# Performance work log

Measured on AMD Instinct MI355X. Metric: run time of the kernel, lower is better.

## Reference

```python
import jax, jax.numpy as jnp
import numpy as np

B, EMB, HID, OUT = 4096, 128, 512, 64
N_SUBPOLICIES = 5
STEPS = N_SUBPOLICIES * 4


def setup_inputs() -> dict:
    key = jax.random.key(0)
    ks = jax.random.split(key, 8)
    s = lambda k, shape: (jax.random.normal(k, shape, jnp.float32) * 0.05)
    return {
        "x": jax.random.randint(ks[0], (B,), 0, OUT),          # initial tokens
        "embedding": s(ks[1], (OUT, EMB)),                      # nn.Embedding weight
        "W_ih": s(ks[2], (4 * HID, EMB)),                       # LSTM input weights (i,f,g,o)
        "W_hh": s(ks[3], (4 * HID, HID)),                       # LSTM recurrent weights
        "b_ih": s(ks[4], (4 * HID,)),
        "b_hh": s(ks[5], (4 * HID,)),
        "W_lin": s(ks[6], (OUT, HID)),                          # nn.Linear weight
        "b_lin": s(ks[7], (OUT,)),
    }


def reference(x, embedding, W_ih, W_hh, b_ih, b_hh, W_lin, b_lin):
    keys = jax.random.split(jax.random.key(42), STEPS)
    h0 = jnp.zeros((x.shape[0], HID), jnp.float32)
    c0 = jnp.zeros_like(h0)
    b = b_ih + b_hh  # fold both LSTM biases once

    def step(carry, k):
        tok, h, c = carry
        e = embedding[tok]                               # [B, EMB]
        gates = e @ W_ih.T + h @ W_hh.T + b              # [B, 4H], torch gate order i,f,g,o
        i, f, g, o = jnp.split(gates, 4, axis=-1)
        c = jax.nn.sigmoid(f) * c + jax.nn.sigmoid(i) * jnp.tanh(g)
        h = jax.nn.sigmoid(o) * jnp.tanh(c)
        logits = h @ W_lin.T + b_lin                     # [B, OUT]
        probs = jax.nn.softmax(logits, axis=-1)
        # torch.multinomial(probs, 1) == categorical sample from logits
        new_tok = jax.random.categorical(k, logits, axis=-1)
        return (new_tok, h, c), probs

    _, probs = jax.lax.scan(step, (x, h0, c0), keys)     # [STEPS, B, OUT]
    return jnp.transpose(probs, (1, 0, 2))               # [B, STEPS, OUT]
```

## Files before the change

kernel.cpp:

```cpp
#include <hip/hip_runtime.h>
#include <stdint.h>
#include <math.h>


#define B_SZ  4096
#define EMB   128
#define HID   512
#define NOUT  64
#define STEPS 20
#define G4    2048
#define HF    ((size_t)B_SZ * HID)

typedef __attribute__((ext_vector_type(8)))  short bf16x8;
typedef __attribute__((ext_vector_type(16))) float f32x16;

union B8 { uint2 q[2]; bf16x8 v; };

__device__ __forceinline__ void tf2x32(uint32_t k0, uint32_t k1,
                                       uint32_t x0, uint32_t x1,
                                       uint32_t& o0, uint32_t& o1) {
  const uint32_t ks2 = k0 ^ k1 ^ 0x1BD11BDAu;
#define TFR(r) { x0 += x1; x1 = (x1 << (r)) | (x1 >> (32 - (r))); x1 ^= x0; }
  x0 += k0; x1 += k1;
  TFR(13) TFR(15) TFR(26) TFR(6)
  x0 += k1;  x1 += ks2 + 1u;
  TFR(17) TFR(29) TFR(16) TFR(24)
  x0 += ks2; x1 += k0 + 2u;
  TFR(13) TFR(15) TFR(26) TFR(6)
  x0 += k0;  x1 += k1 + 3u;
  TFR(17) TFR(29) TFR(16) TFR(24)
  x0 += k1;  x1 += ks2 + 4u;
  TFR(13) TFR(15) TFR(26) TFR(6)
  x0 += ks2; x1 += k0 + 5u;
#undef TFR
  o0 = x0; o1 = x1;
}

__device__ __forceinline__ void bf16split(float f, ushort& hi, ushort& lo) {
  uint32_t u = __float_as_uint(f);
  uint32_t r = u + 0x7fffu + ((u >> 16) & 1u);
  hi = (ushort)(r >> 16);
  float fh = __uint_as_float((r >> 16) << 16);
  float fl = f - fh;
  uint32_t v = __float_as_uint(fl);
  uint32_t r2 = v + 0x7fffu + ((v >> 16) & 1u);
  lo = (ushort)(r2 >> 16);
}

__device__ __forceinline__ void gload_lds16(const ushort* g, ushort* d) {
  __builtin_amdgcn_global_load_lds(
      (const __attribute__((address_space(1))) void*)g,
      (__attribute__((address_space(3))) void*)d, 16, 0, 0);
}

__global__ __launch_bounds__(256) void eproj_kernel(
    const float* __restrict__ emb, const float* __restrict__ W_ih,
    const float* __restrict__ b_ih, const float* __restrict__ b_hh,
    float* __restrict__ E) {
  const int t = blockIdx.x;
  __shared__ float es[EMB];
  for (int k = threadIdx.x; k < EMB; k += blockDim.x) es[k] = emb[t * EMB + k];
  __syncthreads();
  for (int j = threadIdx.x; j < G4; j += blockDim.x) {
    const float* w = W_ih + (size_t)j * EMB;
    float acc = 0.f;
#pragma unroll 8
    for (int k = 0; k < EMB; k += 4) {
      float4 wv = *(const float4*)(w + k);
      acc += wv.x * es[k] + wv.y * es[k + 1] + wv.z * es[k + 2] + wv.w * es[k + 3];
    }
    E[(size_t)t * G4 + j] = acc + b_ih[j] + b_hh[j];
  }
}

__global__ __launch_bounds__(256) void wprep_whh(
    const float* __restrict__ W_hh, ushort* __restrict__ wswz) {
  const int id = blockIdx.x * 256 + threadIdx.x;
  const int ub    = id >> 14;
  const int w14   = id & 16383;
  const int kt    = w14 >> 11;
  const int plane = (w14 >> 10) & 1;
  const int row   = (w14 >> 3) & 127;
  const int ec    = w14 & 7;
  const int grow = (row >> 5) * HID + ub * 32 + (row & 31);
  const int swz = (row & 15) << 2;
  ushort vals[8];
#pragma unroll
  for (int j = 0; j < 8; ++j) {
    const int e = ec * 8 + j;
    const int k = kt * 64 + (e ^ swz);
    ushort hi, lo;
    bf16split(W_hh[(size_t)grow * HID + k], hi, lo);
    vals[j] = plane ? lo : hi;
  }
  *(uint4*)(wswz + (size_t)id * 8) = *(const uint4*)vals;
}

__global__ __launch_bounds__(256) void wprep_lin(
    const float* __restrict__ W_lin, float* __restrict__ wlt) {
  const int id = blockIdx.x * 256 + threadIdx.x;
  const int j = id & 3, o = (id >> 2) & 63, k4 = id >> 8;
  wlt[id] = W_lin[(size_t)o * HID + k4 * 4 + j];
}

__global__ __launch_bounds__(512, 2) void lstm_step_mfma(
    const ushort* __restrict__ hf,
    float*        __restrict__ c,
    float*        __restrict__ h_out,
    ushort*       __restrict__ hf_out,
    const ushort* __restrict__ wswz,
    const float*  __restrict__ E,
    const int*    __restrict__ tok,
    int zh)
{
  __shared__ ushort Bt[2][16384];
  const int tid = threadIdx.x;
  const int w = tid >> 6, l = tid & 63;
  const int l31 = l & 31, lh = l >> 5;

  const int raw = blockIdx.x;
  const int x = raw & 7, j = raw >> 3;
  const int ub  = (x & 3) * 4 + (j & 3);
  const int mbi = (x >> 2) * 8 + (j >> 2);
  const int m0 = mbi * 256 + w * 32;
  const int u0 = ub * 32;

  f32x16 acc[4] = {};

  const size_t abase = ((size_t)(m0 >> 5) * 64 + lh) * 256 + (size_t)l31 * 8;
  const ushort* a0 = hf + abase;
  const ushort* a1 = hf + HF + abase;
  const ushort* wsrc = wswz + (size_t)ub * 131072 + (size_t)(w * 512 + l * 8);

  if (!zh) {
    bf16x8 Aa0[4], Aa1[4], Ab0[4], Ab1[4];

#define SB0 __builtin_amdgcn_sched_barrier(0)
#define STAGE(KT, BUF) { \
  _Pragma("unroll") \
  for (int r = 0; r < 4; ++r) \
    gload_lds16(wsrc + (size_t)(KT) * 16384 + r * 4096, &Bt[BUF][w * 512 + r * 4096]); }
#define LOADA(KT, A0v, A1v) { \
  _Pragma("unroll") \
  for (int kc = 0; kc < 4; ++kc) { \
    const size_t ko = (size_t)((KT) * 8 + kc * 2) * 256; \
    A0v[kc] = *(const bf16x8*)(a0 + ko); \
    A1v[kc] = *(const bf16x8*)(a1 + ko); } }
#define COMPUTE(BUF, A0v, A1v) { \
  __builtin_amdgcn_s_setprio(1); \
  _Pragma("unroll") \
  for (int kc = 0; kc < 4; ++kc) { \
    _Pragma("unroll") \
    for (int s = 0; s < 4; ++s) { \
      const int row = s * 32 + l31; \
      const int swz = (row & 15) << 2; \
      const int eb = kc * 16 + lh * 8; \
      const ushort* rb = &Bt[BUF][row * 64]; \
      B8 uh, ul; \
      uh.q[0] = *(const uint2*)(rb + ((eb)     ^ swz)); \
      uh.q[1] = *(const uint2*)(rb + ((eb + 4) ^ swz)); \
      ul.q[0] = *(const uint2*)(rb + 8192 + ((eb)     ^ swz)); \
      ul.q[1] = *(const uint2*)(rb + 8192 + ((eb + 4) ^ swz)); \
      acc[s] = __builtin_amdgcn_mfma_f32_32x32x16_bf16(A0v[kc], uh.v, acc[s], 0, 0, 0); \
      acc[s] = __builtin_amdgcn_mfma_f32_32x32x16_bf16(A1v[kc], uh.v, acc[s], 0, 0, 0); \
      acc[s] = __builtin_amdgcn_mfma_f32_32x32x16_bf16(A0v[kc], ul.v, acc[s], 0, 0, 0); } } \
  __builtin_amdgcn_s_setprio(0); }
#define FENCE8 { asm volatile("s_waitcnt vmcnt(8)" ::: "memory"); SB0; \
                 __builtin_amdgcn_s_barrier(); }

    STAGE(0, 0); SB0; LOADA(0, Aa0, Aa1); SB0;
    FENCE8;
    STAGE(1, 1); SB0; LOADA(1, Ab0, Ab1); SB0;
    COMPUTE(0, Aa0, Aa1); FENCE8;
    STAGE(2, 0); SB0; LOADA(2, Aa0, Aa1); SB0;
    COMPUTE(1, Ab0, Ab1); FENCE8;
    STAGE(3, 1); SB0; LOADA(3, Ab0, Ab1); SB0;
    COMPUTE(0, Aa0, Aa1); FENCE8;
    STAGE(4, 0); SB0; LOADA(4, Aa0, Aa1); SB0;
    COMPUTE(1, Ab0, Ab1); FENCE8;
    STAGE(5, 1); SB0; LOADA(5, Ab0, Ab1); SB0;
    COMPUTE(0, Aa0, Aa1); FENCE8;
    STAGE(6, 0); SB0; LOADA(6, Aa0, Aa1); SB0;
    COMPUTE(1, Ab0, Ab1); FENCE8;
    STAGE(7, 1); SB0; LOADA(7, Ab0, Ab1); SB0;
    COMPUTE(0, Aa0, Aa1); FENCE8;
    COMPUTE(1, Ab0, Ab1);
#undef FENCE8
#undef COMPUTE
#undef LOADA
#undef STAGE
#undef SB0
  }

  const int u = u0 + l31;
#pragma unroll
  for (int r = 0; r < 16; ++r) {
    const int m = m0 + (r & 3) + 8 * (r >> 2) + 4 * lh;
    const int tk = tok[m];
    const float* Erow = E + (size_t)tk * G4;
    const float gi = acc[0][r] + Erow[u];
    const float gf = acc[1][r] + Erow[HID + u];
    const float gg = acc[2][r] + Erow[2 * HID + u];
    const float go = acc[3][r] + Erow[3 * HID + u];
    const float si = 1.f / (1.f + expf(-gi));
    const float sf = 1.f / (1.f + expf(-gf));
    const float so = 1.f / (1.f + expf(-go));
    const size_t ci = (size_t)m * HID + u;
    const float cv = zh ? 0.f : c[ci];
    const float nc = sf * cv + si * tanhf(gg);
    const float hv = so * tanhf(nc);
    c[ci] = nc;
    h_out[ci] = hv;
    ushort hi, lo;
    bf16split(hv, hi, lo);
    const size_t fo = ((size_t)(m >> 5) * 64 + (u >> 3)) * 256 + (size_t)(m & 31) * 8 + (u & 7);
    hf_out[fo] = hi;
    hf_out[HF + fo] = lo;
  }
}

__global__ __launch_bounds__(256) void logits2(
    const float* __restrict__ h, const float* __restrict__ wlt,
    const float* __restrict__ b_lin, float* __restrict__ out,
    int* __restrict__ tok, int step)
{
  const int tid = threadIdx.x;
  const int o = tid & 63;
  const int rg = tid >> 6;
  const int b0 = blockIdx.x * 8 + rg * 2;
  float acc0 = 0.f, acc1 = 0.f;
  const float* h0 = h + (size_t)b0 * HID;
  const float* h1 = h0 + HID;
#pragma unroll 4
  for (int k4 = 0; k4 < 128; ++k4) {
    const float4 wv = *(const float4*)(wlt + (size_t)(k4 * 64 + o) * 4);
    const float4 x0 = *(const float4*)(h0 + k4 * 4);
    const float4 x1 = *(const float4*)(h1 + k4 * 4);
    acc0 += wv.x * x0.x + wv.y * x0.y + wv.z * x0.z + wv.w * x0.w;
    acc1 += wv.x * x1.x + wv.y * x1.y + wv.z * x1.z + wv.w * x1.w;
  }
  const float bl = b_lin[o];
  uint32_t s0, s1;
  tf2x32(0u, 42u, 0u, (uint32_t)step, s0, s1);
  float lg[2] = {acc0 + bl, acc1 + bl};
#pragma unroll
  for (int r = 0; r < 2; ++r) {
    const int b = b0 + r;
    const float logit = lg[r];
    float mx = logit;
#pragma unroll
    for (int d = 32; d; d >>= 1) mx = fmaxf(mx, __shfl_xor(mx, d));
    float e = expf(logit - mx);
    float ssum = e;
#pragma unroll
    for (int d = 32; d; d >>= 1) ssum += __shfl_xor(ssum, d);
    out[((size_t)b * STEPS + step) * NOUT + o] = e / ssum;

    uint32_t r0, r1;
    tf2x32(s0, s1, 0u, (uint32_t)(b * NOUT + o), r0, r1);
    const uint32_t bits = r0 ^ r1;
    float uu = __uint_as_float((bits >> 9) | 0x3f800000u) - 1.0f;
    uu = fmaxf(uu, 1.17549435e-38f);
    const float gmb = -logf(-logf(uu));
    float v = logit + gmb;
    int bi = o;
#pragma unroll
    for (int d = 32; d; d >>= 1) {
      float ov = __shfl_xor(v, d);
      int oi = __shfl_xor(bi, d);
      if (ov > v || (ov == v && oi < bi)) { v = ov; bi = oi; }
    }
    if (o == 0) tok[b] = bi;
  }
}

extern "C" void kernel_launch(void* const* d_in, const int* in_sizes, int n_in,
                              void* d_out, int out_size, void* d_ws, size_t ws_size,
                              hipStream_t stream) {
  const int*   x     = (const int*)d_in[0];
  const float* emb   = (const float*)d_in[1];
  const float* W_ih  = (const float*)d_in[2];
  const float* W_hh  = (const float*)d_in[3];
  const float* b_ih  = (const float*)d_in[4];
  const float* b_hh  = (const float*)d_in[5];
  const float* W_lin = (const float*)d_in[6];
  const float* b_lin = (const float*)d_in[7];
  float* out = (float*)d_out;

  float*  E    = (float*)d_ws;
  float*  c    = E + 131072;
  float*  h    = c + HF;
  float*  wlt  = h + HF;
  ushort* hf0  = (ushort*)(wlt + 32768);
  ushort* hf1  = hf0 + 2 * HF;
  ushort* wswz = hf1 + 2 * HF;
  int*    tok  = (int*)(wswz + 2097152);

  eproj_kernel<<<64, 256, 0, stream>>>(emb, W_ih, b_ih, b_hh, E);
  wprep_whh<<<1024, 256, 0, stream>>>(W_hh, wswz);
  wprep_lin<<<128, 256, 0, stream>>>(W_lin, wlt);

  const int* cur_tok = x;
  ushort* hfin = hf0;
  ushort* hfout = hf1;
  for (int t = 0; t < STEPS; ++t) {
    lstm_step_mfma<<<256, 512, 0, stream>>>(hfin, c, h, hfout, wswz, E, cur_tok, t == 0);
    logits2<<<512, 256, 0, stream>>>(h, wlt, b_lin, out, tok, t);
    cur_tok = tok;
    ushort* tmp = hfin; hfin = hfout; hfout = tmp;
  }
}
```

Before: 1.326 ms.

## Fuse all LSTM steps and logits into one persistent kernel with grid barriers

Replaces the 40 per-step kernel launches (LSTM step plus logits/sampling) with a single persistent kernel of 256 blocks. Blocks synchronise through a global atomic grid barrier, and the cell state now lives in registers instead of global memory. Sigmoid and tanh switch to fast exp/rcp approximations. This removes launch overhead and the c-state round trips. In exchange it depends on all 256 blocks being co-resident, adds two grid barriers per step, and the approximate activations may change numerics slightly.

```diff
diff --git a/kernel.cpp b/kernel.cpp
--- a/kernel.cpp
+++ b/kernel.cpp
@@ -10,6 +10,7 @@
 #define STEPS 20
 #define G4    2048
 #define HF    ((size_t)B_SZ * HID)
+#define NBLK  256
 
 typedef __attribute__((ext_vector_type(8)))  short bf16x8;
 typedef __attribute__((ext_vector_type(16))) float f32x16;
@@ -53,6 +54,31 @@
       (__attribute__((address_space(3))) void*)d, 16, 0, 0);
 }
 
+__device__ __forceinline__ float fsig(float x) {
+  return __builtin_amdgcn_rcpf(1.f + __expf(-x));
+}
+__device__ __forceinline__ float ftanh(float x) {
+  return 1.f - 2.f * __builtin_amdgcn_rcpf(1.f + __expf(2.f * x));
+}
+
+__device__ __forceinline__ void gridbar(unsigned* cnt, unsigned* gen) {
+  __syncthreads();
+  if (threadIdx.x == 0) {
+    __threadfence();
+    unsigned g = __hip_atomic_load(gen, __ATOMIC_RELAXED, __HIP_MEMORY_SCOPE_AGENT);
+    unsigned a = __hip_atomic_fetch_add(cnt, 1u, __ATOMIC_ACQ_REL, __HIP_MEMORY_SCOPE_AGENT);
+    if (a == NBLK - 1) {
+      __hip_atomic_store(cnt, 0u, __ATOMIC_RELAXED, __HIP_MEMORY_SCOPE_AGENT);
+      __hip_atomic_fetch_add(gen, 1u, __ATOMIC_RELEASE, __HIP_MEMORY_SCOPE_AGENT);
+    } else {
+      while (__hip_atomic_load(gen, __ATOMIC_ACQUIRE, __HIP_MEMORY_SCOPE_AGENT) == g)
+        __builtin_amdgcn_s_sleep(2);
+    }
+  }
+  __syncthreads();
+  __threadfence();
+}
+
 __global__ __launch_bounds__(256) void eproj_kernel(
     const float* __restrict__ emb, const float* __restrict__ W_ih,
     const float* __restrict__ b_ih, const float* __restrict__ b_hh,
@@ -103,15 +129,18 @@
   wlt[id] = W_lin[(size_t)o * HID + k4 * 4 + j];
 }
 
-__global__ __launch_bounds__(512, 2) void lstm_step_mfma(
-    const ushort* __restrict__ hf,
-    float*        __restrict__ c,
-    float*        __restrict__ h_out,
-    ushort*       __restrict__ hf_out,
+__global__ __launch_bounds__(512, 2) void ctrl_persist(
+    const int*    __restrict__ x,
     const ushort* __restrict__ wswz,
     const float*  __restrict__ E,
-    const int*    __restrict__ tok,
-    int zh)
+    const float*  __restrict__ wlt,
+    const float*  __restrict__ b_lin,
+    float*        __restrict__ h_out,
+    ushort*       __restrict__ hf0,
+    ushort*       __restrict__ hf1,
+    int*          __restrict__ tok,
+    float*        __restrict__ out,
+    unsigned*     __restrict__ bar)
 {
   __shared__ ushort Bt[2][16384];
   const int tid = threadIdx.x;
@@ -119,27 +148,36 @@
   const int l31 = l & 31, lh = l >> 5;
 
   const int raw = blockIdx.x;
-  const int x = raw & 7, j = raw >> 3;
-  const int ub  = (x & 3) * 4 + (j & 3);
-  const int mbi = (x >> 2) * 8 + (j >> 2);
+  const int xq = raw & 7, jq = raw >> 3;
+  const int ub  = (xq & 3) * 4 + (jq & 3);
+  const int mbi = (xq >> 2) * 8 + (jq >> 2);
   const int m0 = mbi * 256 + w * 32;
   const int u0 = ub * 32;
-
-  f32x16 acc[4] = {};
-
-  const size_t abase = ((size_t)(m0 >> 5) * 64 + lh) * 256 + (size_t)l31 * 8;
-  const ushort* a0 = hf + abase;
-  const ushort* a1 = hf + HF + abase;
+  const int u  = u0 + l31;
+
   const ushort* wsrc = wswz + (size_t)ub * 131072 + (size_t)(w * 512 + l * 8);
-
-  if (!zh) {
-    bf16x8 Aa0[4], Aa1[4], Ab0[4], Ab1[4];
+  const int lb0 = raw * 16 + w * 2;
+
+  f32x16 creg = {};
+
+  for (int t = 0; t < STEPS; ++t) {
+    const ushort* hin  = (t & 1) ? hf1 : hf0;
+    ushort*       hout = (t & 1) ? hf0 : hf1;
+    const int*    tk   = t ? tok : x;
+
+    f32x16 acc[4] = {};
+
+    if (t > 0) {
+      const size_t abase = ((size_t)(m0 >> 5) * 64 + lh) * 256 + (size_t)l31 * 8;
+      const ushort* a0 = hin + abase;
+      const ushort* a1 = hin + HF + abase;
+      bf16x8 Aa0[4], Aa1[4], Ab0[4], Ab1[4];
 
 #define SB0 __builtin_amdgcn_sched_barrier(0)
 #define STAGE(KT, BUF) { \
   _Pragma("unroll") \
-  for (int r = 0; r < 4; ++r) \
-    gload_lds16(wsrc + (size_t)(KT) * 16384 + r * 4096, &Bt[BUF][w * 512 + r * 4096]); }
+  for (int rr = 0; rr < 4; ++rr) \
+    gload_lds16(wsrc + (size_t)(KT) * 16384 + rr * 4096, &Bt[BUF][w * 512 + rr * 4096]); }
 #define LOADA(KT, A0v, A1v) { \
   _Pragma("unroll") \
   for (int kc = 0; kc < 4; ++kc) { \
@@ -168,109 +206,104 @@
 #define FENCE8 { asm volatile("s_waitcnt vmcnt(8)" ::: "memory"); SB0; \
                  __builtin_amdgcn_s_barrier(); }
 
-    STAGE(0, 0); SB0; LOADA(0, Aa0, Aa1); SB0;
-    FENCE8;
-    STAGE(1, 1); SB0; LOADA(1, Ab0, Ab1); SB0;
-    COMPUTE(0, Aa0, Aa1); FENCE8;
-    STAGE(2, 0); SB0; LOADA(2, Aa0, Aa1); SB0;
-    COMPUTE(1, Ab0, Ab1); FENCE8;
-    STAGE(3, 1); SB0; LOADA(3, Ab0, Ab1); SB0;
-    COMPUTE(0, Aa0, Aa1); FENCE8;
-    STAGE(4, 0); SB0; LOADA(4, Aa0, Aa1); SB0;
-    COMPUTE(1, Ab0, Ab1); FENCE8;
-    STAGE(5, 1); SB0; LOADA(5, Ab0, Ab1); SB0;
-    COMPUTE(0, Aa0, Aa1); FENCE8;
-    STAGE(6, 0); SB0; LOADA(6, Aa0, Aa1); SB0;
-    COMPUTE(1, Ab0, Ab1); FENCE8;
-    STAGE(7, 1); SB0; LOADA(7, Ab0, Ab1); SB0;
-    COMPUTE(0, Aa0, Aa1); FENCE8;
-    COMPUTE(1, Ab0, Ab1);
+      STAGE(0, 0); SB0; LOADA(0, Aa0, Aa1); SB0;
+      FENCE8;
+      STAGE(1, 1); SB0; LOADA(1, Ab0, Ab1); SB0;
+      COMPUTE(0, Aa0, Aa1); FENCE8;
+      STAGE(2, 0); SB0; LOADA(2, Aa0, Aa1); SB0;
+      COMPUTE(1, Ab0, Ab1); FENCE8;
+      STAGE(3, 1); SB0; LOADA(3, Ab0, Ab1); SB0;
+      COMPUTE(0, Aa0, Aa1); FENCE8;
+      STAGE(4, 0); SB0; LOADA(4, Aa0, Aa1); SB0;
+      COMPUTE(1, Ab0, Ab1); FENCE8;
+      STAGE(5, 1); SB0; LOADA(5, Ab0, Ab1); SB0;
+      COMPUTE(0, Aa0, Aa1); FENCE8;
+      STAGE(6, 0); SB0; LOADA(6, Aa0, Aa1); SB0;
+      COMPUTE(1, Ab0, Ab1); FENCE8;
+      STAGE(7, 1); SB0; LOADA(7, Ab0, Ab1); SB0;
+      COMPUTE(0, Aa0, Aa1); FENCE8;
+      COMPUTE(1, Ab0, Ab1);
 #undef FENCE8
 #undef COMPUTE
 #undef LOADA
 #undef STAGE
 #undef SB0
-  }
-
-  const int u = u0 + l31;
-#pragma unroll
-  for (int r = 0; r < 16; ++r) {
-    const int m = m0 + (r & 3) + 8 * (r >> 2) + 4 * lh;
-    const int tk = tok[m];
-    const float* Erow = E + (size_t)tk * G4;
-    const float gi = acc[0][r] + Erow[u];
-    const float gf = acc[1][r] + Erow[HID + u];
-    const float gg = acc[2][r] + Erow[2 * HID + u];
-    const float go = acc[3][r] + Erow[3 * HID + u];
-    const float si = 1.f / (1.f + expf(-gi));
-    const float sf = 1.f / (1.f + expf(-gf));
-    const float so = 1.f / (1.f + expf(-go));
-    const size_t ci = (size_t)m * HID + u;
-    const float cv = zh ? 0.f : c[ci];
-    const float nc = sf * cv + si * tanhf(gg);
-    const float hv = so * tanhf(nc);
-    c[ci] = nc;
-    h_out[ci] = hv;
-    ushort hi, lo;
-    bf16split(hv, hi, lo);
-    const size_t fo = ((size_t)(m >> 5) * 64 + (u >> 3)) * 256 + (size_t)(m & 31) * 8 + (u & 7);
-    hf_out[fo] = hi;
-    hf_out[HF + fo] = lo;
-  }
-}
-
-__global__ __launch_bounds__(256) void logits2(
-    const float* __restrict__ h, const float* __restrict__ wlt,
-    const float* __restrict__ b_lin, float* __restrict__ out,
-    int* __restrict__ tok, int step)
-{
-  const int tid = threadIdx.x;
-  const int o = tid & 63;
-  const int rg = tid >> 6;
-  const int b0 = blockIdx.x * 8 + rg * 2;
-  float acc0 = 0.f, acc1 = 0.f;
-  const float* h0 = h + (size_t)b0 * HID;
-  const float* h1 = h0 + HID;
+    }
+
+#pragma unroll
+    for (int r = 0; r < 16; ++r) {
+      const int m = m0 + (r & 3) + 8 * (r >> 2) + 4 * lh;
+      const int tv = tk[m];
+      const float* Erow = E + (size_t)tv * G4;
+      const float gi = acc[0][r] + Erow[u];
+      const float gf = acc[1][r] + Erow[HID + u];
+      const float gg = acc[2][r] + Erow[2 * HID + u];
+      const float go = acc[3][r] + Erow[3 * HID + u];
+      const float si = fsig(gi);
+      const float sf = fsig(gf);
+      const float so = fsig(go);
+      const float nc = sf * creg[r] + si * ftanh(gg);
+      creg[r] = nc;
+      const float hv = so * ftanh(nc);
+      h_out[(size_t)m * HID + u] = hv;
+      ushort hi, lo;
+      bf16split(hv, hi, lo);
+      const size_t fo = ((size_t)(m >> 5) * 64 + (u >> 3)) * 256 + (size_t)(m & 31) * 8 + (u & 7);
+      hout[fo] = hi;
+      hout[HF + fo] = lo;
+    }
+
+    gridbar(bar, bar + 1);
+
+    {
+      const int o = l;
+      float acc0 = 0.f, acc1 = 0.f;
+      const float* h0p = h_out + (size_t)lb0 * HID;
+      const float* h1p = h0p + HID;
 #pragma unroll 4
-  for (int k4 = 0; k4 < 128; ++k4) {
-    const float4 wv = *(const float4*)(wlt + (size_t)(k4 * 64 + o) * 4);
-    const float4 x0 = *(const float4*)(h0 + k4 * 4);
-    const float4 x1 = *(const float4*)(h1 + k4 * 4);
-    acc0 += wv.x * x0.x + wv.y * x0.y + wv.z * x0.z + wv.w * x0.w;
-    acc1 += wv.x * x1.x + wv.y * x1.y + wv.z * x1.z + wv.w * x1.w;
-  }
-  const float bl = b_lin[o];
-  uint32_t s0, s1;
-  tf2x32(0u, 42u, 0u, (uint32_t)step, s0, s1);
-  float lg[2] = {acc0 + bl, acc1 + bl};
-#pragma unroll
-  for (int r = 0; r < 2; ++r) {
-    const int b = b0 + r;
-    const float logit = lg[r];
-    float mx = logit;
-#pragma unroll
-    for (int d = 32; d; d >>= 1) mx = fmaxf(mx, __shfl_xor(mx, d));
-    float e = expf(logit - mx);
-    float ssum = e;
-#pragma unroll
-    for (int d = 32; d; d >>= 1) ssum += __shfl_xor(ssum, d);
-    out[((size_t)b * STEPS + step) * NOUT + o] = e / ssum;
-
-    uint32_t r0, r1;
-    tf2x32(s0, s1, 0u, (uint32_t)(b * NOUT + o), r0, r1);
-    const uint32_t bits = r0 ^ r1;
-    float uu = __uint_as_float((bits >> 9) | 0x3f800000u) - 1.0f;
-    uu = fmaxf(uu, 1.17549435e-38f);
-    const float gmb = -logf(-logf(uu));
-    float v = logit + gmb;
-    int bi = o;
-#pragma unroll
-    for (int d = 32; d; d >>= 1) {
-      float ov = __shfl_xor(v, d);
-      int oi = __shfl_xor(bi, d);
-      if (ov > v || (ov == v && oi < bi)) { v = ov; bi = oi; }
-    }
-    if (o == 0) tok[b] = bi;
+      for (int k4 = 0; k4 < 128; ++k4) {
+        const float4 wv = *(const float4*)(wlt + (size_t)(k4 * 64 + o) * 4);
+        const float4 x0 = *(const float4*)(h0p + k4 * 4);
+        const float4 x1 = *(const float4*)(h1p + k4 * 4);
+        acc0 += wv.x * x0.x + wv.y * x0.y + wv.z * x0.z + wv.w * x0.w;
+        acc1 += wv.x * x1.x + wv.y * x1.y + wv.z * x1.z + wv.w * x1.w;
+      }
+      const float bl = b_lin[o];
+      uint32_t s0, s1;
+      tf2x32(0u, 42u, 0u, (uint32_t)t, s0, s1);
+      float lg[2] = {acc0 + bl, acc1 + bl};
+#pragma unroll
+      for (int r = 0; r < 2; ++r) {
+        const int b = lb0 + r;
+        const float logit = lg[r];
+        float mx = logit;
+#pragma unroll
+        for (int d = 32; d; d >>= 1) mx = fmaxf(mx, __shfl_xor(mx, d));
+        float e = expf(logit - mx);
+        float ssum = e;
+#pragma unroll
+        for (int d = 32; d; d >>= 1) ssum += __shfl_xor(ssum, d);
+        out[((size_t)b * STEPS + t) * NOUT + o] = e / ssum;
+
+        uint32_t r0, r1;
+        tf2x32(s0, s1, 0u, (uint32_t)(b * NOUT + o), r0, r1);
+        const uint32_t bits = r0 ^ r1;
+        float uu = __uint_as_float((bits >> 9) | 0x3f800000u) - 1.0f;
+        uu = fmaxf(uu, 1.17549435e-38f);
+        const float gmb = -logf(-logf(uu));
+        float v = logit + gmb;
+        int bi = o;
+#pragma unroll
+        for (int d = 32; d; d >>= 1) {
+          float ov = __shfl_xor(v, d);
+          int oi = __shfl_xor(bi, d);
+          if (ov > v || (ov == v && oi < bi)) { v = ov; bi = oi; }
+        }
+        if (o == 0) tok[b] = bi;
+      }
+    }
+
+    gridbar(bar, bar + 1);
   }
 }
 
@@ -288,25 +321,20 @@
   float* out = (float*)d_out;
 
   float*  E    = (float*)d_ws;
-  float*  c    = E + 131072;
-  float*  h    = c + HF;
+  float*  h    = E + 131072;
   float*  wlt  = h + HF;
   ushort* hf0  = (ushort*)(wlt + 32768);
   ushort* hf1  = hf0 + 2 * HF;
   ushort* wswz = hf1 + 2 * HF;
   int*    tok  = (int*)(wswz + 2097152);
+  unsigned* bar = (unsigned*)(tok + B_SZ);
+
+  hipMemsetAsync(bar, 0, 2 * sizeof(unsigned), stream);
 
   eproj_kernel<<<64, 256, 0, stream>>>(emb, W_ih, b_ih, b_hh, E);
   wprep_whh<<<1024, 256, 0, stream>>>(W_hh, wswz);
   wprep_lin<<<128, 256, 0, stream>>>(W_lin, wlt);
 
-  const int* cur_tok = x;
-  ushort* hfin = hf0;
-  ushort* hfout = hf1;
-  for (int t = 0; t < STEPS; ++t) {
-    lstm_step_mfma<<<256, 512, 0, stream>>>(hfin, c, h, hfout, wswz, E, cur_tok, t == 0);
-    logits2<<<512, 256, 0, stream>>>(h, wlt, b_lin, out, tok, t);
-    cur_tok = tok;
-    ushort* tmp = hfin; hfin = hfout; hfout = tmp;
-  }
-}
+  ctrl_persist<<<NBLK, 512, 0, stream>>>(x, wswz, E, wlt, b_lin,
+                                         h, hf0, hf1, tok, out, bar);
+}
```

Result: slower. 3.885 ms (+193.1%).
